# Kernel tuning notes

Hardware: AMD Instinct MI355X
Metric: run time of the kernel (lower is better)

Reference implementation:

```python
import jax, jax.numpy as jnp
import numpy as np

N = 50000   # nodes
E = 600000  # edges
D = 128     # in_channels == heads*hidden_channels
OUT = 64    # out_channels
L = 3       # local_layers
EPS = 1e-5  # BatchNorm eps


def setup_inputs() -> dict:
    key = jax.random.key(0)
    ks = jax.random.split(key, 10)
    s = 0.05
    x = jax.random.normal(ks[0], (N, D), jnp.float32)
    edge_index = jax.random.randint(ks[1], (2, E), 0, N, dtype=jnp.int32)
    Wg = jax.random.normal(ks[2], (L, D, D), jnp.float32) * s  # GCNConv weights
    bg = jnp.zeros((L, D), jnp.float32)                         # GCNConv biases
    Wl = jax.random.normal(ks[3], (L, D, D), jnp.float32) * s  # residual Linear weights
    bl = jax.random.normal(ks[4], (L, D), jnp.float32) * s
    gamma = jnp.ones((L, D), jnp.float32)                       # BN scale
    beta = jnp.zeros((L, D), jnp.float32)                       # BN shift
    Wp = jax.random.normal(ks[5], (D, OUT), jnp.float32) * s   # pred head
    bp = jnp.zeros((OUT,), jnp.float32)
    return {"x": x, "edge_index": edge_index, "Wg": Wg, "bg": bg,
            "Wl": Wl, "bl": bl, "gamma": gamma, "beta": beta,
            "Wp": Wp, "bp": bp}


def reference(x, edge_index, Wg, bg, Wl, bl, gamma, beta, Wp, bp):
    src, dst = edge_index[0], edge_index[1]
    # GCN symmetric normalization with self-loops (PyG gcn_norm):
    # deg computed on target (col) including self-loop.
    deg = jax.ops.segment_sum(jnp.ones((E,), x.dtype), dst, num_segments=N) + 1.0
    dinv = jax.lax.rsqrt(deg)                      # deg^{-1/2}, [N]
    enorm = dinv[src] * dinv[dst]                  # per-edge norm, [E]
    self_norm = (dinv * dinv)[:, None]             # deg^{-1} for self-loop, [N,1]

    h = x
    x_local = jnp.zeros((N, D), x.dtype)
    for i in range(L):
        hg = h @ Wg[i]                             # [N, D] transformed features
        # gather -> weight -> scatter-add (message passing) + self-loop term
        agg = jax.ops.segment_sum(hg[src] * enorm[:, None], dst, num_segments=N)
        conv = agg + hg * self_norm + bg[i]
        # residual linear
        h = conv + h @ Wl[i] + bl[i]
        # BatchNorm1d (training-mode batch statistics, biased var)
        mu = jnp.mean(h, axis=0)
        var = jnp.mean(jnp.square(h - mu), axis=0)
        h = (h - mu) * jax.lax.rsqrt(var + EPS) * gamma[i] + beta[i]
        h = jax.nn.relu(h)
        x_local = x_local + h                      # add_ accumulation
    return x_local @ Wp + bp
```

## Files before the change

kernel.cpp:

```cpp
#include <hip/hip_runtime.h>

#define D 128
#define OUTC 64
#define EC 256

typedef float floatx4 __attribute__((ext_vector_type(4)));
typedef short short8 __attribute__((ext_vector_type(8)));

__device__ inline unsigned short f2bf(float f) {
  unsigned int u = __float_as_uint(f);
  unsigned int r = (u + 0x7FFF + ((u >> 16) & 1)) >> 16;
  return (unsigned short)r;
}

__device__ inline int swz(int row, int k) { return row * 128 + (k ^ ((row & 7) << 3)); }

__global__ __launch_bounds__(256) void k_prepx(const float* __restrict__ x, unsigned short* __restrict__ xb, int total4) {
  int stride = gridDim.x * blockDim.x;
  for (int i = blockIdx.x * blockDim.x + threadIdx.x; i < total4; i += stride) {
    float4 v = ((const float4*)x)[i];
    ushort4 o;
    o.x = f2bf(v.x); o.y = f2bf(v.y); o.z = f2bf(v.z); o.w = f2bf(v.w);
    ((ushort4*)xb)[i] = o;
  }
}

__global__ __launch_bounds__(256) void k_prepw(const float* __restrict__ Wg, const float* __restrict__ Wl,
                                               const float* __restrict__ Wp,
                                               unsigned short* __restrict__ Wgt, unsigned short* __restrict__ Wlt,
                                               unsigned short* __restrict__ Wpt) {
  int u = blockIdx.x * 256 + threadIdx.x;
  const int W1 = 3 * D * D;
  if (u < W1) {
    int i = u / (D * D), rem = u % (D * D);
    int k = rem / D, n = rem % D;
    Wgt[i * D * D + n * D + k] = f2bf(Wg[u]);
  } else if (u < 2 * W1) {
    int v = u - W1;
    int i = v / (D * D), rem = v % (D * D);
    int k = rem / D, n = rem % D;
    Wlt[i * D * D + n * D + k] = f2bf(Wl[v]);
  } else if (u < 2 * W1 + D * OUTC) {
    int v = u - 2 * W1;
    int k = v / OUTC, n = v % OUTC;
    Wpt[n * D + k] = f2bf(Wp[v]);
  }
}


__global__ __launch_bounds__(256) void k_bh(const int* __restrict__ dst, int* __restrict__ bh,
                                            int E, int nbuk, int chk) {
  __shared__ int hist[256];
  int t = threadIdx.x, c = blockIdx.x;
  hist[t] = 0;
  __syncthreads();
  int s = c * chk, e = min(E, s + chk);
  for (int j = s + t; j < e; j += 256)
    atomicAdd(&hist[dst[j] >> 8], 1);
  __syncthreads();
  if (t < nbuk) bh[t * EC + c] = hist[t];
}

__device__ inline int block_scan4(int4 v, int t, int* total) {
  int s = v.x + v.y + v.z + v.w;
  int lane = t & 63, w = t >> 6;
  int incl = s;
  #pragma unroll
  for (int off = 1; off < 64; off <<= 1) {
    int nb = __shfl_up(incl, off);
    if (lane >= off) incl += nb;
  }
  __shared__ int wsum[4];
  if (lane == 63) wsum[w] = incl;
  __syncthreads();
  int woff = 0;
  #pragma unroll
  for (int k = 0; k < 3; ++k) if (w > k) woff += wsum[k];
  if (total) *total = wsum[0] + wsum[1] + wsum[2] + wsum[3];
  return woff + incl - s;
}

__global__ __launch_bounds__(256) void k_gscan1(int* __restrict__ arr, int* __restrict__ bsum, int n) {
  int t = threadIdx.x;
  int i0 = blockIdx.x * 1024 + t * 4;
  int4 v = make_int4(0, 0, 0, 0);
  if (i0 + 3 < n) v = *(const int4*)(arr + i0);
  else {
    if (i0 < n) v.x = arr[i0];
    if (i0 + 1 < n) v.y = arr[i0 + 1];
    if (i0 + 2 < n) v.z = arr[i0 + 2];
    if (i0 + 3 < n) v.w = arr[i0 + 3];
  }
  int total;
  int e = block_scan4(v, t, &total);
  if (i0 < n) {
    int4 o;
    o.x = e; o.y = e + v.x; o.z = o.y + v.y; o.w = o.z + v.z;
    if (i0 + 3 < n) *(int4*)(arr + i0) = o;
    else {
      arr[i0] = o.x;
      if (i0 + 1 < n) arr[i0 + 1] = o.y;
      if (i0 + 2 < n) arr[i0 + 2] = o.z;
    }
  }
  if (t == 0) bsum[blockIdx.x] = total;
}

__global__ __launch_bounds__(256) void k_gscan2(int* __restrict__ bsum, int nb) {
  int t = threadIdx.x;
  int i0 = t * 4;
  int4 v = make_int4(0, 0, 0, 0);
  if (i0 + 3 < nb) v = *(const int4*)(bsum + i0);
  else {
    if (i0 < nb) v.x = bsum[i0];
    if (i0 + 1 < nb) v.y = bsum[i0 + 1];
    if (i0 + 2 < nb) v.z = bsum[i0 + 2];
    if (i0 + 3 < nb) v.w = bsum[i0 + 3];
  }
  int e = block_scan4(v, t, nullptr);
  if (i0 < nb) {
    bsum[i0] = e;
    if (i0 + 1 < nb) bsum[i0 + 1] = e + v.x;
    if (i0 + 2 < nb) bsum[i0 + 2] = e + v.x + v.y;
    if (i0 + 3 < nb) bsum[i0 + 3] = e + v.x + v.y + v.z;
  }
}

__global__ __launch_bounds__(256) void k_scatter(const int* __restrict__ src, const int* __restrict__ dst,
                                                 const int* __restrict__ bhs, const int* __restrict__ bsum,
                                                 int2* __restrict__ ebuk, int E, int nbuk, int chk) {
  __shared__ int cur[256];
  int t = threadIdx.x, c = blockIdx.x;
  if (t < nbuk) {
    int idx = t * EC + c;
    cur[t] = bhs[idx] + bsum[idx >> 10];
  }
  __syncthreads();
  int s = c * chk, e = min(E, s + chk);
  for (int j = s + t; j < e; j += 256) {
    int d = dst[j];
    int pos = atomicAdd(&cur[d >> 8], 1);
    ebuk[pos] = make_int2(src[j], d);
  }
}

__global__ __launch_bounds__(256) void k_csr(const int2* __restrict__ ebuk, const int* __restrict__ bhs,
                                             const int* __restrict__ bsum,
                                             int* __restrict__ rowstart, int* __restrict__ csr,
                                             float* __restrict__ dinv, int E, int N, int nbuk) {
  __shared__ int cnt[256];
  __shared__ int wsum[4];
  int t = threadIdx.x, b = blockIdx.x;
  int si = b * EC;
  int s = bhs[si] + bsum[si >> 10];
  int e;
  if (b + 1 < nbuk) { int ei_ = (b + 1) * EC; e = bhs[ei_] + bsum[ei_ >> 10]; }
  else e = E;
  cnt[t] = 0;
  __syncthreads();
  for (int j = s + t; j < e; j += 256)
    atomicAdd(&cnt[ebuk[j].y & 255], 1);
  __syncthreads();
  int v = cnt[t];
  int lane = t & 63, w = t >> 6;
  int incl = v;
  #pragma unroll
  for (int off = 1; off < 64; off <<= 1) {
    int nb = __shfl_up(incl, off);
    if (lane >= off) incl += nb;
  }
  if (lane == 63) wsum[w] = incl;
  __syncthreads();
  int woff = 0;
  #pragma unroll
  for (int k = 0; k < 3; ++k) if (w > k) woff += wsum[k];
  int rs = s + woff + incl - v;
  int node = (b << 8) + t;
  __syncthreads();
  cnt[t] = rs;
  if (node < N) {
    rowstart[node] = rs;
    dinv[node] = rsqrtf((float)v + 1.0f);
  }
  if (node == 0) rowstart[N] = E;
  __syncthreads();
  for (int j = s + t; j < e; j += 256) {
    int2 ed = ebuk[j];
    int pos = atomicAdd(&cnt[ed.y & 255], 1);
    csr[pos] = ed.x;
  }
}

__global__ __launch_bounds__(256) void k_dual(const unsigned short* __restrict__ Ab,
                                              const unsigned short* __restrict__ Wgt,
                                              const unsigned short* __restrict__ Wlt,
                                              const float* __restrict__ bg, const float* __restrict__ bl,
                                              unsigned short* __restrict__ hg, float* __restrict__ hl, int M) {
  __shared__ unsigned short As[64 * 128];
  __shared__ unsigned short Bs[128 * 128];
  int tid = threadIdx.x;
  int row0 = blockIdx.x * 64;

  {
    int r = tid >> 2;
    int row = row0 + r;
    const unsigned short* src = Ab + (size_t)row * D;
    #pragma unroll
    for (int j = 0; j < 4; ++j) {
      int c = (tid & 3) + j * 4;
      short8 v = {0, 0, 0, 0, 0, 0, 0, 0};
      if (row < M) v = *(const short8*)(src + c * 8);
      *(short8*)&As[swz(r, c * 8)] = v;
    }
  }
  #pragma unroll
  for (int j = 0; j < 8; ++j) {
    int idx = tid + j * 256;
    int nr = idx >> 4, c = idx & 15;
    *(short8*)&Bs[swz(nr, c * 8)] = *(const short8*)(Wgt + nr * D + c * 8);
  }
  __syncthreads();

  int lane = tid & 63, w = tid >> 6;
  int lrow = lane & 15, lk = (lane >> 4) * 8;

  short8 af[4][4];
  #pragma unroll
  for (int m = 0; m < 4; ++m) {
    int ar = lrow + m * 16;
    #pragma unroll
    for (int kk = 0; kk < 4; ++kk)
      af[m][kk] = *(const short8*)&As[swz(ar, lk + kk * 32)];
  }

  {
    short8 bfg[2][4];
    #pragma unroll
    for (int n = 0; n < 2; ++n) {
      int br = w * 32 + n * 16 + lrow;
      #pragma unroll
      for (int kk = 0; kk < 4; ++kk)
        bfg[n][kk] = *(const short8*)&Bs[swz(br, lk + kk * 32)];
    }
    floatx4 acc[4][2];
    #pragma unroll
    for (int m = 0; m < 4; ++m)
      #pragma unroll
      for (int n = 0; n < 2; ++n)
        acc[m][n] = (floatx4)0.0f;
    #pragma unroll
    for (int kk = 0; kk < 4; ++kk)
      #pragma unroll
      for (int m = 0; m < 4; ++m)
        #pragma unroll
        for (int n = 0; n < 2; ++n)
          acc[m][n] = __builtin_amdgcn_mfma_f32_16x16x32_bf16(af[m][kk], bfg[n][kk], acc[m][n], 0, 0, 0);
    #pragma unroll
    for (int m = 0; m < 4; ++m)
      #pragma unroll
      for (int n = 0; n < 2; ++n) {
        int col = w * 32 + n * 16 + lrow;
        #pragma unroll
        for (int reg = 0; reg < 4; ++reg) {
          int row = row0 + m * 16 + (lane >> 4) * 4 + reg;
          if (row < M) hg[(size_t)row * D + col] = f2bf(acc[m][n][reg]);
        }
      }
  }
  __syncthreads();
  #pragma unroll
  for (int j = 0; j < 8; ++j) {
    int idx = tid + j * 256;
    int nr = idx >> 4, c = idx & 15;
    *(short8*)&Bs[swz(nr, c * 8)] = *(const short8*)(Wlt + nr * D + c * 8);
  }
  __syncthreads();
  {
    short8 bfl[2][4];
    #pragma unroll
    for (int n = 0; n < 2; ++n) {
      int br = w * 32 + n * 16 + lrow;
      #pragma unroll
      for (int kk = 0; kk < 4; ++kk)
        bfl[n][kk] = *(const short8*)&Bs[swz(br, lk + kk * 32)];
    }
    floatx4 acc[4][2];
    #pragma unroll
    for (int m = 0; m < 4; ++m)
      #pragma unroll
      for (int n = 0; n < 2; ++n)
        acc[m][n] = (floatx4)0.0f;
    #pragma unroll
    for (int kk = 0; kk < 4; ++kk)
      #pragma unroll
      for (int m = 0; m < 4; ++m)
        #pragma unroll
        for (int n = 0; n < 2; ++n)
          acc[m][n] = __builtin_amdgcn_mfma_f32_16x16x32_bf16(af[m][kk], bfl[n][kk], acc[m][n], 0, 0, 0);
    #pragma unroll
    for (int m = 0; m < 4; ++m)
      #pragma unroll
      for (int n = 0; n < 2; ++n) {
        int col = w * 32 + n * 16 + lrow;
        float bias = bg[col] + bl[col];
        #pragma unroll
        for (int reg = 0; reg < 4; ++reg) {
          int row = row0 + m * 16 + (lane >> 4) * 4 + reg;
          if (row < M) hl[(size_t)row * D + col] = acc[m][n][reg] + bias;
        }
      }
  }
}

__global__ __launch_bounds__(256) void k_agg(const unsigned short* __restrict__ hg, float* __restrict__ pre,
                                             const int* __restrict__ rowstart, const int* __restrict__ csr,
                                             const float* __restrict__ dinv,
                                             float* __restrict__ partial, int n, int ABS) {
  int t = threadIdx.x, b = blockIdx.x;
  int w = t >> 6, lane = t & 63;
  const unsigned int* base = (const unsigned int*)hg;
  float st_s0 = 0.f, st_s1 = 0.f, st_q0 = 0.f, st_q1 = 0.f;
  int c = lane * 2;
  int node0 = b * 16 + w * 4;
  #pragma unroll 1
  for (int k = 0; k < 4; ++k) {
    int node = node0 + k;
    if (node >= n) break;
    int s = rowstart[node], e = rowstart[node + 1];
    float dn = dinv[node];
    unsigned int ps = base[(size_t)node * 64 + lane];
    float* pp = pre + (size_t)node * D;
    float2 old = *(const float2*)(pp + c);
    float a0 = 0.f, a1 = 0.f, b0 = 0.f, b1 = 0.f;
    float c0 = 0.f, c1 = 0.f, d0 = 0.f, d1 = 0.f;
    int j = s;
    for (; j + 4 <= e; j += 4) {
      int sn0 = csr[j], sn1 = csr[j + 1], sn2 = csr[j + 2], sn3 = csr[j + 3];
      float w0 = dinv[sn0], w1 = dinv[sn1], w2 = dinv[sn2], w3 = dinv[sn3];
      unsigned int p0 = base[(size_t)sn0 * 64 + lane];
      unsigned int p1 = base[(size_t)sn1 * 64 + lane];
      unsigned int p2 = base[(size_t)sn2 * 64 + lane];
      unsigned int p3 = base[(size_t)sn3 * 64 + lane];
      a0 += w0 * __uint_as_float(p0 << 16); a1 += w0 * __uint_as_float(p0 & 0xFFFF0000u);
      b0 += w1 * __uint_as_float(p1 << 16); b1 += w1 * __uint_as_float(p1 & 0xFFFF0000u);
      c0 += w2 * __uint_as_float(p2 << 16); c1 += w2 * __uint_as_float(p2 & 0xFFFF0000u);
      d0 += w3 * __uint_as_float(p3 << 16); d1 += w3 * __uint_as_float(p3 & 0xFFFF0000u);
    }
    for (; j < e; ++j) {
      int sn = csr[j];
      float wv = dinv[sn];
      unsigned int p = base[(size_t)sn * 64 + lane];
      a0 += wv * __uint_as_float(p << 16);
      a1 += wv * __uint_as_float(p & 0xFFFF0000u);
    }
    float acc0 = (a0 + b0) + (c0 + d0);
    float acc1 = (a1 + b1) + (c1 + d1);
    float sf = dn * dn;
    float h0 = __uint_as_float(ps << 16);
    float h1 = __uint_as_float(ps & 0xFFFF0000u);
    float p0 = dn * acc0 + h0 * sf + old.x;
    float p1 = dn * acc1 + h1 * sf + old.y;
    *(float2*)(pp + c) = make_float2(p0, p1);
    st_s0 += p0; st_s1 += p1;
    st_q0 += p0 * p0; st_q1 += p1 * p1;
  }
  __shared__ float sm[4][128], sq[4][128];
  sm[w][c] = st_s0; sm[w][c + 1] = st_s1;
  sq[w][c] = st_q0; sq[w][c + 1] = st_q1;
  __syncthreads();
  if (t < 128) {
    float s = (sm[0][t] + sm[1][t]) + (sm[2][t] + sm[3][t]);
    float q = (sq[0][t] + sq[1][t]) + (sq[2][t] + sq[3][t]);
    partial[(size_t)t * ABS + b] = s;
    partial[(size_t)(128 + t) * ABS + b] = q;
  }
}

__global__ __launch_bounds__(256) void k_fin2(const float* __restrict__ partial,
                                              const float* __restrict__ gamma, const float* __restrict__ beta,
                                              float* __restrict__ ab, int nab, int ABS, float invN) {
  int cch = blockIdx.x;
  int t = threadIdx.x;
  const float* ps = partial + (size_t)cch * ABS;
  const float* pq = partial + (size_t)(128 + cch) * ABS;
  float s = 0.f, q = 0.f;
  for (int i = t; i < nab; i += 256) { s += ps[i]; q += pq[i]; }
  __shared__ float rs[256], rq[256];
  rs[t] = s; rq[t] = q;
  __syncthreads();
  if (t < 64) {
    s = (rs[t] + rs[t + 64]) + (rs[t + 128] + rs[t + 192]);
    q = (rq[t] + rq[t + 64]) + (rq[t + 128] + rq[t + 192]);
    #pragma unroll
    for (int off = 32; off; off >>= 1) {
      s += __shfl_down(s, off);
      q += __shfl_down(q, off);
    }
    if (t == 0) {
      float mean = s * invN;
      float var = q * invN - mean * mean;
      float inv = rsqrtf(var + 1e-5f);
      float g = gamma[cch];
      ab[cch] = g * inv;
      ab[128 + cch] = beta[cch] - mean * inv * g;
    }
  }
}

template<bool FIRST>
__global__ __launch_bounds__(256) void k_fused(const float* __restrict__ pre, const float* __restrict__ ab,
                                               const unsigned short* __restrict__ Wpt, const float* __restrict__ bp,
                                               const unsigned short* __restrict__ Wgt,
                                               const unsigned short* __restrict__ Wlt,
                                               const float* __restrict__ bgn, const float* __restrict__ bln,
                                               float* __restrict__ out, unsigned short* __restrict__ hg,
                                               float* __restrict__ hl, int M) {
  __shared__ unsigned short As[64 * 128];
  __shared__ unsigned short Bs[128 * 128];
  int tid = threadIdx.x;
  int row0 = blockIdx.x * 64;

  {
    int r = tid >> 2, qq = tid & 3;
    int row = row0 + r;
    bool valid = row < M;
    const float* Pp = pre + (size_t)row * D;
    #pragma unroll
    for (int ch = 0; ch < 4; ++ch) {
      int k0 = qq * 32 + ch * 8;
      float4 p0 = make_float4(0.f, 0.f, 0.f, 0.f), p1 = p0;
      if (valid) { p0 = *(const float4*)(Pp + k0); p1 = *(const float4*)(Pp + k0 + 4); }
      float4 a0 = *(const float4*)(ab + k0),        a1 = *(const float4*)(ab + k0 + 4);
      float4 b0 = *(const float4*)(ab + 128 + k0),  b1 = *(const float4*)(ab + 128 + k0 + 4);
      unsigned short hv[8];
      hv[0] = f2bf(fmaxf(p0.x * a0.x + b0.x, 0.f));
      hv[1] = f2bf(fmaxf(p0.y * a0.y + b0.y, 0.f));
      hv[2] = f2bf(fmaxf(p0.z * a0.z + b0.z, 0.f));
      hv[3] = f2bf(fmaxf(p0.w * a0.w + b0.w, 0.f));
      hv[4] = f2bf(fmaxf(p1.x * a1.x + b1.x, 0.f));
      hv[5] = f2bf(fmaxf(p1.y * a1.y + b1.y, 0.f));
      hv[6] = f2bf(fmaxf(p1.z * a1.z + b1.z, 0.f));
      hv[7] = f2bf(fmaxf(p1.w * a1.w + b1.w, 0.f));
      *(short8*)&As[swz(r, k0)] = *(const short8*)hv;
    }
  }
  #pragma unroll
  for (int j = 0; j < 4; ++j) {
    int idx = tid + j * 256;
    int nr = idx >> 4, c = idx & 15;
    *(short8*)&Bs[swz(nr, c * 8)] = *(const short8*)(Wpt + nr * D + c * 8);
  }
  __syncthreads();

  int lane = tid & 63, w = tid >> 6;
  int lrow = lane & 15, lk = (lane >> 4) * 8;

  short8 af[4][4];
  #pragma unroll
  for (int m = 0; m < 4; ++m) {
    int ar = lrow + m * 16;
    #pragma unroll
    for (int kk = 0; kk < 4; ++kk)
      af[m][kk] = *(const short8*)&As[swz(ar, lk + kk * 32)];
  }

  {
    short8 bfr[4];
    int br = w * 16 + lrow;
    #pragma unroll
    for (int kk = 0; kk < 4; ++kk)
      bfr[kk] = *(const short8*)&Bs[swz(br, lk + kk * 32)];
    floatx4 acc[4];
    #pragma unroll
    for (int m = 0; m < 4; ++m) acc[m] = (floatx4)0.0f;
    #pragma unroll
    for (int kk = 0; kk < 4; ++kk)
      #pragma unroll
      for (int m = 0; m < 4; ++m)
        acc[m] = __builtin_amdgcn_mfma_f32_16x16x32_bf16(af[m][kk], bfr[kk], acc[m], 0, 0, 0);
    int col = w * 16 + lrow;
    float bpv = FIRST ? bp[col] : 0.f;
    #pragma unroll
    for (int m = 0; m < 4; ++m)
      #pragma unroll
      for (int reg = 0; reg < 4; ++reg) {
        int row = row0 + m * 16 + (lane >> 4) * 4 + reg;
        if (row < M) {
          float* op = &out[(size_t)row * OUTC + col];
          float v = acc[m][reg] + bpv;
          if (!FIRST) v += *op;
          *op = v;
        }
      }
  }
  __syncthreads();
  #pragma unroll
  for (int j = 0; j < 8; ++j) {
    int idx = tid + j * 256;
    int nr = idx >> 4, c = idx & 15;
    *(short8*)&Bs[swz(nr, c * 8)] = *(const short8*)(Wgt + nr * D + c * 8);
  }
  __syncthreads();
  {
    short8 bfg[2][4];
    #pragma unroll
    for (int n = 0; n < 2; ++n) {
      int br = w * 32 + n * 16 + lrow;
      #pragma unroll
      for (int kk = 0; kk < 4; ++kk)
        bfg[n][kk] = *(const short8*)&Bs[swz(br, lk + kk * 32)];
    }
    floatx4 acc[4][2];
    #pragma unroll
    for (int m = 0; m < 4; ++m)
      #pragma unroll
      for (int n = 0; n < 2; ++n)
        acc[m][n] = (floatx4)0.0f;
    #pragma unroll
    for (int kk = 0; kk < 4; ++kk)
      #pragma unroll
      for (int m = 0; m < 4; ++m)
        #pragma unroll
        for (int n = 0; n < 2; ++n)
          acc[m][n] = __builtin_amdgcn_mfma_f32_16x16x32_bf16(af[m][kk], bfg[n][kk], acc[m][n], 0, 0, 0);
    #pragma unroll
    for (int m = 0; m < 4; ++m)
      #pragma unroll
      for (int n = 0; n < 2; ++n) {
        int col = w * 32 + n * 16 + lrow;
        #pragma unroll
        for (int reg = 0; reg < 4; ++reg) {
          int row = row0 + m * 16 + (lane >> 4) * 4 + reg;
          if (row < M) hg[(size_t)row * D + col] = f2bf(acc[m][n][reg]);
        }
      }
  }
  __syncthreads();
  #pragma unroll
  for (int j = 0; j < 8; ++j) {
    int idx = tid + j * 256;
    int nr = idx >> 4, c = idx & 15;
    *(short8*)&Bs[swz(nr, c * 8)] = *(const short8*)(Wlt + nr * D + c * 8);
  }
  __syncthreads();
  {
    short8 bfl[2][4];
    #pragma unroll
    for (int n = 0; n < 2; ++n) {
      int br = w * 32 + n * 16 + lrow;
      #pragma unroll
      for (int kk = 0; kk < 4; ++kk)
        bfl[n][kk] = *(const short8*)&Bs[swz(br, lk + kk * 32)];
    }
    floatx4 acc[4][2];
    #pragma unroll
    for (int m = 0; m < 4; ++m)
      #pragma unroll
      for (int n = 0; n < 2; ++n)
        acc[m][n] = (floatx4)0.0f;
    #pragma unroll
    for (int kk = 0; kk < 4; ++kk)
      #pragma unroll
      for (int m = 0; m < 4; ++m)
        #pragma unroll
        for (int n = 0; n < 2; ++n)
          acc[m][n] = __builtin_amdgcn_mfma_f32_16x16x32_bf16(af[m][kk], bfl[n][kk], acc[m][n], 0, 0, 0);
    #pragma unroll
    for (int m = 0; m < 4; ++m)
      #pragma unroll
      for (int n = 0; n < 2; ++n) {
        int col = w * 32 + n * 16 + lrow;
        float bias = bgn[col] + bln[col];
        #pragma unroll
        for (int reg = 0; reg < 4; ++reg) {
          int row = row0 + m * 16 + (lane >> 4) * 4 + reg;
          if (row < M) hl[(size_t)row * D + col] = acc[m][n][reg] + bias;
        }
      }
  }
}

__global__ __launch_bounds__(256) void k_out(const float* __restrict__ pre, const float* __restrict__ ab,
                                             const unsigned short* __restrict__ Wpt,
                                             float* __restrict__ out, int M) {
  __shared__ unsigned short As[64 * 128];
  __shared__ unsigned short Bs[OUTC * 128];
  int tid = threadIdx.x;
  int row0 = blockIdx.x * 64;

  {
    int r = tid >> 2, qq = tid & 3;
    int row = row0 + r;
    bool valid = row < M;
    const float* Pp = pre + (size_t)row * D;
    #pragma unroll
    for (int ch = 0; ch < 4; ++ch) {
      int k0 = qq * 32 + ch * 8;
      float4 p0 = make_float4(0.f, 0.f, 0.f, 0.f), p1 = p0;
      if (valid) { p0 = *(const float4*)(Pp + k0); p1 = *(const float4*)(Pp + k0 + 4); }
      float4 a0 = *(const float4*)(ab + k0),        a1 = *(const float4*)(ab + k0 + 4);
      float4 b0 = *(const float4*)(ab + 128 + k0),  b1 = *(const float4*)(ab + 128 + k0 + 4);
      unsigned short hv[8];
      hv[0] = f2bf(fmaxf(p0.x * a0.x + b0.x, 0.f));
      hv[1] = f2bf(fmaxf(p0.y * a0.y + b0.y, 0.f));
      hv[2] = f2bf(fmaxf(p0.z * a0.z + b0.z, 0.f));
      hv[3] = f2bf(fmaxf(p0.w * a0.w + b0.w, 0.f));
      hv[4] = f2bf(fmaxf(p1.x * a1.x + b1.x, 0.f));
      hv[5] = f2bf(fmaxf(p1.y * a1.y + b1.y, 0.f));
      hv[6] = f2bf(fmaxf(p1.z * a1.z + b1.z, 0.f));
      hv[7] = f2bf(fmaxf(p1.w * a1.w + b1.w, 0.f));
      *(short8*)&As[swz(r, k0)] = *(const short8*)hv;
    }
  }
  #pragma unroll
  for (int j = 0; j < 4; ++j) {
    int idx = tid + j * 256;
    int nr = idx >> 4, c = idx & 15;
    *(short8*)&Bs[swz(nr, c * 8)] = *(const short8*)(Wpt + nr * D + c * 8);
  }
  __syncthreads();

  int lane = tid & 63, w = tid >> 6;
  int lrow = lane & 15, lk = (lane >> 4) * 8;

  short8 af[4][4];
  #pragma unroll
  for (int m = 0; m < 4; ++m) {
    int ar = lrow + m * 16;
    #pragma unroll
    for (int kk = 0; kk < 4; ++kk)
      af[m][kk] = *(const short8*)&As[swz(ar, lk + kk * 32)];
  }
  short8 bfr[4];
  {
    int br = w * 16 + lrow;
    #pragma unroll
    for (int kk = 0; kk < 4; ++kk)
      bfr[kk] = *(const short8*)&Bs[swz(br, lk + kk * 32)];
  }
  floatx4 acc[4];
  #pragma unroll
  for (int m = 0; m < 4; ++m) acc[m] = (floatx4)0.0f;
  #pragma unroll
  for (int kk = 0; kk < 4; ++kk)
    #pragma unroll
    for (int m = 0; m < 4; ++m)
      acc[m] = __builtin_amdgcn_mfma_f32_16x16x32_bf16(af[m][kk], bfr[kk], acc[m], 0, 0, 0);

  int col = w * 16 + lrow;
  #pragma unroll
  for (int m = 0; m < 4; ++m)
    #pragma unroll
    for (int reg = 0; reg < 4; ++reg) {
      int row = row0 + m * 16 + (lane >> 4) * 4 + reg;
      if (row < M) {
        float* op = &out[(size_t)row * OUTC + col];
        *op = *op + acc[m][reg];
      }
    }
}

extern "C" void kernel_launch(void* const* d_in, const int* in_sizes, int n_in,
                              void* d_out, int out_size, void* d_ws, size_t ws_size,
                              hipStream_t stream) {
  const float* x     = (const float*)d_in[0];
  const int*   ei    = (const int*)d_in[1];
  const float* Wg    = (const float*)d_in[2];
  const float* bg    = (const float*)d_in[3];
  const float* Wl    = (const float*)d_in[4];
  const float* bl    = (const float*)d_in[5];
  const float* gamma = (const float*)d_in[6];
  const float* beta  = (const float*)d_in[7];
  const float* Wp    = (const float*)d_in[8];
  const float* bp    = (const float*)d_in[9];
  float* out = (float*)d_out;

  int N = in_sizes[0] / D;
  int E = in_sizes[1] / 2;
  const int* srcp = ei;
  const int* dstp = ei + E;

  char* wsb = (char*)d_ws;
  size_t off = 0;
  auto alloc = [&](size_t bytes) {
    off = (off + 255) & ~(size_t)255;
    void* p = wsb + off;
    off += bytes;
    return p;
  };
  int nab = (N + 15) / 16;
  int ABS = (nab + 63) & ~63;
  float* dinv     = (float*)alloc((size_t)N * 4);
  int*   rowstart = (int*)alloc((size_t)(N + 1) * 4);
  int*   csr      = (int*)alloc((size_t)E * 4);
  int*   bh       = (int*)alloc((size_t)256 * EC * 4);
  int2*  ebuk     = (int2*)alloc((size_t)E * 8);
  int*   bsum     = (int*)alloc(1024 * 4);
  float* partial  = (float*)alloc((size_t)256 * ABS * 4);
  float* ab       = (float*)alloc(3 * 256 * 4);
  unsigned short* xb  = (unsigned short*)alloc((size_t)N * D * 2);
  unsigned short* hg  = (unsigned short*)alloc((size_t)N * D * 2);
  float* hl       = (float*)alloc((size_t)N * D * 4);
  unsigned short* Wgt = (unsigned short*)alloc(3 * D * D * 2);
  unsigned short* Wlt = (unsigned short*)alloc(3 * D * D * 2);
  unsigned short* Wpt = (unsigned short*)alloc(D * OUTC * 2);
  (void)ws_size; (void)n_in; (void)out_size;

  k_prepx<<<1024, 256, 0, stream>>>(x, xb, N * D / 4);
  int wtotal = 2 * 3 * D * D + D * OUTC;
  k_prepw<<<(wtotal + 255) / 256, 256, 0, stream>>>(Wg, Wl, Wp, Wgt, Wlt, Wpt);

  int nbuk = (N + 255) >> 8;
  int chk  = (E + EC - 1) / EC;
  k_bh<<<EC, 256, 0, stream>>>(dstp, bh, E, nbuk, chk);
  int sn  = nbuk * EC;
  int snb = (sn + 1023) >> 10;
  k_gscan1<<<snb, 256, 0, stream>>>(bh, bsum, sn);
  k_gscan2<<<1, 256, 0, stream>>>(bsum, snb);
  k_scatter<<<EC, 256, 0, stream>>>(srcp, dstp, bh, bsum, ebuk, E, nbuk, chk);
  k_csr<<<nbuk, 256, 0, stream>>>(ebuk, bh, bsum, rowstart, csr, dinv, E, N, nbuk);

  int mt = (N + 63) / 64;
  float invN = 1.0f / (float)N;

  k_dual<<<mt, 256, 0, stream>>>(xb, Wgt, Wlt, bg, bl, hg, hl, N);

  for (int i = 0; i < 3; ++i) {
    k_agg<<<nab, 256, 0, stream>>>(hg, hl, rowstart, csr, dinv, partial, N, ABS);
    k_fin2<<<128, 256, 0, stream>>>(partial, gamma + (size_t)i * D, beta + (size_t)i * D,
                                    ab + i * 256, nab, ABS, invN);
    if (i == 0)
      k_fused<true><<<mt, 256, 0, stream>>>(hl, ab + i * 256, Wpt, bp,
                                            Wgt + (size_t)(i + 1) * D * D, Wlt + (size_t)(i + 1) * D * D,
                                            bg + (size_t)(i + 1) * D, bl + (size_t)(i + 1) * D,
                                            out, hg, hl, N);
    else if (i == 1)
      k_fused<false><<<mt, 256, 0, stream>>>(hl, ab + i * 256, Wpt, bp,
                                             Wgt + (size_t)(i + 1) * D * D, Wlt + (size_t)(i + 1) * D * D,
                                             bg + (size_t)(i + 1) * D, bl + (size_t)(i + 1) * D,
                                             out, hg, hl, N);
    else
      k_out<<<mt, 256, 0, stream>>>(hl, ab + i * 256, Wpt, out, N);
  }
}
```

Measured before the change: 290.8 us.

## Store residual/pre-activation buffer in bf16 and pack edge buckets into 32-bit words

The residual-linear output buffer (hl/pre) is now stored as bf16 instead of fp32, halving its traffic in the dual GEMM epilogue, the aggregation read-modify-write, and the fused/out prologues. Edge bucket entries are packed into a single 32-bit word (24-bit src plus 8-bit local dst), halving scatter/CSR-build traffic. The aggregation kernel handles 2 nodes per wave instead of 4, doubling the block count. Risks: extra rounding in the pre-BN activations, and src indices are limited to 24 bits.

```diff
diff --git a/kernel.cpp b/kernel.cpp
--- a/kernel.cpp
+++ b/kernel.cpp
@@ -11,6 +11,9 @@
   unsigned int u = __float_as_uint(f);
   unsigned int r = (u + 0x7FFF + ((u >> 16) & 1)) >> 16;
   return (unsigned short)r;
+}
+__device__ inline float bf2f(unsigned short u) {
+  return __uint_as_float(((unsigned int)u) << 16);
 }
 
 __device__ inline int swz(int row, int k) { return row * 128 + (k ^ ((row & 7) << 3)); }
@@ -128,7 +131,7 @@
 
 __global__ __launch_bounds__(256) void k_scatter(const int* __restrict__ src, const int* __restrict__ dst,
                                                  const int* __restrict__ bhs, const int* __restrict__ bsum,
-                                                 int2* __restrict__ ebuk, int E, int nbuk, int chk) {
+                                                 unsigned int* __restrict__ ebuk, int E, int nbuk, int chk) {
   __shared__ int cur[256];
   int t = threadIdx.x, c = blockIdx.x;
   if (t < nbuk) {
@@ -140,11 +143,11 @@
   for (int j = s + t; j < e; j += 256) {
     int d = dst[j];
     int pos = atomicAdd(&cur[d >> 8], 1);
-    ebuk[pos] = make_int2(src[j], d);
-  }
-}
-
-__global__ __launch_bounds__(256) void k_csr(const int2* __restrict__ ebuk, const int* __restrict__ bhs,
+    ebuk[pos] = (unsigned int)src[j] | ((unsigned int)(d & 255) << 24);
+  }
+}
+
+__global__ __launch_bounds__(256) void k_csr(const unsigned int* __restrict__ ebuk, const int* __restrict__ bhs,
                                              const int* __restrict__ bsum,
                                              int* __restrict__ rowstart, int* __restrict__ csr,
                                              float* __restrict__ dinv, int E, int N, int nbuk) {
@@ -159,7 +162,7 @@
   cnt[t] = 0;
   __syncthreads();
   for (int j = s + t; j < e; j += 256)
-    atomicAdd(&cnt[ebuk[j].y & 255], 1);
+    atomicAdd(&cnt[ebuk[j] >> 24], 1);
   __syncthreads();
   int v = cnt[t];
   int lane = t & 63, w = t >> 6;
@@ -185,9 +188,9 @@
   if (node == 0) rowstart[N] = E;
   __syncthreads();
   for (int j = s + t; j < e; j += 256) {
-    int2 ed = ebuk[j];
-    int pos = atomicAdd(&cnt[ed.y & 255], 1);
-    csr[pos] = ed.x;
+    unsigned int ed = ebuk[j];
+    int pos = atomicAdd(&cnt[ed >> 24], 1);
+    csr[pos] = (int)(ed & 0xFFFFFFu);
   }
 }
 
@@ -195,7 +198,7 @@
                                               const unsigned short* __restrict__ Wgt,
                                               const unsigned short* __restrict__ Wlt,
                                               const float* __restrict__ bg, const float* __restrict__ bl,
-                                              unsigned short* __restrict__ hg, float* __restrict__ hl, int M) {
+                                              unsigned short* __restrict__ hg, unsigned short* __restrict__ hl, int M) {
   __shared__ unsigned short As[64 * 128];
   __shared__ unsigned short Bs[128 * 128];
   int tid = threadIdx.x;
@@ -306,31 +309,31 @@
         #pragma unroll
         for (int reg = 0; reg < 4; ++reg) {
           int row = row0 + m * 16 + (lane >> 4) * 4 + reg;
-          if (row < M) hl[(size_t)row * D + col] = acc[m][n][reg] + bias;
+          if (row < M) hl[(size_t)row * D + col] = f2bf(acc[m][n][reg] + bias);
         }
       }
   }
 }
 
-__global__ __launch_bounds__(256) void k_agg(const unsigned short* __restrict__ hg, float* __restrict__ pre,
+__global__ __launch_bounds__(256) void k_agg(const unsigned short* __restrict__ hg, unsigned short* __restrict__ pre,
                                              const int* __restrict__ rowstart, const int* __restrict__ csr,
                                              const float* __restrict__ dinv,
                                              float* __restrict__ partial, int n, int ABS) {
   int t = threadIdx.x, b = blockIdx.x;
   int w = t >> 6, lane = t & 63;
   const unsigned int* base = (const unsigned int*)hg;
+  unsigned int* prew = (unsigned int*)pre;
   float st_s0 = 0.f, st_s1 = 0.f, st_q0 = 0.f, st_q1 = 0.f;
   int c = lane * 2;
-  int node0 = b * 16 + w * 4;
+  int node0 = b * 8 + w * 2;
   #pragma unroll 1
-  for (int k = 0; k < 4; ++k) {
+  for (int k = 0; k < 2; ++k) {
     int node = node0 + k;
     if (node >= n) break;
     int s = rowstart[node], e = rowstart[node + 1];
     float dn = dinv[node];
     unsigned int ps = base[(size_t)node * 64 + lane];
-    float* pp = pre + (size_t)node * D;
-    float2 old = *(const float2*)(pp + c);
+    unsigned int oldw = prew[(size_t)node * 64 + lane];
     float a0 = 0.f, a1 = 0.f, b0 = 0.f, b1 = 0.f;
     float c0 = 0.f, c1 = 0.f, d0 = 0.f, d1 = 0.f;
     int j = s;
@@ -358,9 +361,11 @@
     float sf = dn * dn;
     float h0 = __uint_as_float(ps << 16);
     float h1 = __uint_as_float(ps & 0xFFFF0000u);
-    float p0 = dn * acc0 + h0 * sf + old.x;
-    float p1 = dn * acc1 + h1 * sf + old.y;
-    *(float2*)(pp + c) = make_float2(p0, p1);
+    float old0 = __uint_as_float(oldw << 16);
+    float old1 = __uint_as_float(oldw & 0xFFFF0000u);
+    float p0 = dn * acc0 + h0 * sf + old0;
+    float p1 = dn * acc1 + h1 * sf + old1;
+    prew[(size_t)node * 64 + lane] = (unsigned int)f2bf(p0) | ((unsigned int)f2bf(p1) << 16);
     st_s0 += p0; st_s1 += p1;
     st_q0 += p0 * p0; st_q1 += p1 * p1;
   }
@@ -408,13 +413,13 @@
 }
 
 template<bool FIRST>
-__global__ __launch_bounds__(256) void k_fused(const float* __restrict__ pre, const float* __restrict__ ab,
+__global__ __launch_bounds__(256) void k_fused(const unsigned short* __restrict__ pre, const float* __restrict__ ab,
                                                const unsigned short* __restrict__ Wpt, const float* __restrict__ bp,
                                                const unsigned short* __restrict__ Wgt,
                                                const unsigned short* __restrict__ Wlt,
                                                const float* __restrict__ bgn, const float* __restrict__ bln,
                                                float* __restrict__ out, unsigned short* __restrict__ hg,
-                                               float* __restrict__ hl, int M) {
+                                               unsigned short* __restrict__ hl, int M) {
   __shared__ unsigned short As[64 * 128];
   __shared__ unsigned short Bs[128 * 128];
   int tid = threadIdx.x;
@@ -424,23 +429,22 @@
     int r = tid >> 2, qq = tid & 3;
     int row = row0 + r;
     bool valid = row < M;
-    const float* Pp = pre + (size_t)row * D;
+    const unsigned short* Pp = pre + (size_t)row * D;
     #pragma unroll
     for (int ch = 0; ch < 4; ++ch) {
       int k0 = qq * 32 + ch * 8;
-      float4 p0 = make_float4(0.f, 0.f, 0.f, 0.f), p1 = p0;
-      if (valid) { p0 = *(const float4*)(Pp + k0); p1 = *(const float4*)(Pp + k0 + 4); }
+      short8 pv = {0, 0, 0, 0, 0, 0, 0, 0};
+      if (valid) pv = *(const short8*)(Pp + k0);
       float4 a0 = *(const float4*)(ab + k0),        a1 = *(const float4*)(ab + k0 + 4);
       float4 b0 = *(const float4*)(ab + 128 + k0),  b1 = *(const float4*)(ab + 128 + k0 + 4);
+      float av[8] = {a0.x, a0.y, a0.z, a0.w, a1.x, a1.y, a1.z, a1.w};
+      float bv[8] = {b0.x, b0.y, b0.z, b0.w, b1.x, b1.y, b1.z, b1.w};
       unsigned short hv[8];
-      hv[0] = f2bf(fmaxf(p0.x * a0.x + b0.x, 0.f));
-      hv[1] = f2bf(fmaxf(p0.y * a0.y + b0.y, 0.f));
-      hv[2] = f2bf(fmaxf(p0.z * a0.z + b0.z, 0.f));
-      hv[3] = f2bf(fmaxf(p0.w * a0.w + b0.w, 0.f));
-      hv[4] = f2bf(fmaxf(p1.x * a1.x + b1.x, 0.f));
-      hv[5] = f2bf(fmaxf(p1.y * a1.y + b1.y, 0.f));
-      hv[6] = f2bf(fmaxf(p1.z * a1.z + b1.z, 0.f));
-      hv[7] = f2bf(fmaxf(p1.w * a1.w + b1.w, 0.f));
+      #pragma unroll
+      for (int jj = 0; jj < 8; ++jj) {
+        float f = bf2f((unsigned short)pv[jj]);
+        hv[jj] = f2bf(fmaxf(f * av[jj] + bv[jj], 0.f));
+      }
       *(short8*)&As[swz(r, k0)] = *(const short8*)hv;
     }
   }
@@ -574,13 +578,13 @@
         #pragma unroll
         for (int reg = 0; reg < 4; ++reg) {
           int row = row0 + m * 16 + (lane >> 4) * 4 + reg;
-          if (row < M) hl[(size_t)row * D + col] = acc[m][n][reg] + bias;
+          if (row < M) hl[(size_t)row * D + col] = f2bf(acc[m][n][reg] + bias);
         }
       }
   }
 }
 
-__global__ __launch_bounds__(256) void k_out(const float* __restrict__ pre, const float* __restrict__ ab,
+__global__ __launch_bounds__(256) void k_out(const unsigned short* __restrict__ pre, const float* __restrict__ ab,
                                              const unsigned short* __restrict__ Wpt,
                                              float* __restrict__ out, int M) {
   __shared__ unsigned short As[64 * 128];
@@ -592,23 +596,22 @@
     int r = tid >> 2, qq = tid & 3;
     int row = row0 + r;
     bool valid = row < M;
-    const float* Pp = pre + (size_t)row * D;
+    const unsigned short* Pp = pre + (size_t)row * D;
     #pragma unroll
     for (int ch = 0; ch < 4; ++ch) {
       int k0 = qq * 32 + ch * 8;
-      float4 p0 = make_float4(0.f, 0.f, 0.f, 0.f), p1 = p0;
-      if (valid) { p0 = *(const float4*)(Pp + k0); p1 = *(const float4*)(Pp + k0 + 4); }
+      short8 pv = {0, 0, 0, 0, 0, 0, 0, 0};
+      if (valid) pv = *(const short8*)(Pp + k0);
       float4 a0 = *(const float4*)(ab + k0),        a1 = *(const float4*)(ab + k0 + 4);
       float4 b0 = *(const float4*)(ab + 128 + k0),  b1 = *(const float4*)(ab + 128 + k0 + 4);
+      float av[8] = {a0.x, a0.y, a0.z, a0.w, a1.x, a1.y, a1.z, a1.w};
+      float bv[8] = {b0.x, b0.y, b0.z, b0.w, b1.x, b1.y, b1.z, b1.w};
       unsigned short hv[8];
-      hv[0] = f2bf(fmaxf(p0.x * a0.x + b0.x, 0.f));
-      hv[1] = f2bf(fmaxf(p0.y * a0.y + b0.y, 0.f));
-      hv[2] = f2bf(fmaxf(p0.z * a0.z + b0.z, 0.f));
-      hv[3] = f2bf(fmaxf(p0.w * a0.w + b0.w, 0.f));
-      hv[4] = f2bf(fmaxf(p1.x * a1.x + b1.x, 0.f));
-      hv[5] = f2bf(fmaxf(p1.y * a1.y + b1.y, 0.f));
-      hv[6] = f2bf(fmaxf(p1.z * a1.z + b1.z, 0.f));
-      hv[7] = f2bf(fmaxf(p1.w * a1.w + b1.w, 0.f));
+      #pragma unroll
+      for (int jj = 0; jj < 8; ++jj) {
+        float f = bf2f((unsigned short)pv[jj]);
+        hv[jj] = f2bf(fmaxf(f * av[jj] + bv[jj], 0.f));
+      }
       *(short8*)&As[swz(r, k0)] = *(const short8*)hv;
     }
   }
@@ -688,19 +691,19 @@
     off += bytes;
     return p;
   };
-  int nab = (N + 15) / 16;
+  int nab = (N + 7) / 8;
   int ABS = (nab + 63) & ~63;
   float* dinv     = (float*)alloc((size_t)N * 4);
   int*   rowstart = (int*)alloc((size_t)(N + 1) * 4);
   int*   csr      = (int*)alloc((size_t)E * 4);
   int*   bh       = (int*)alloc((size_t)256 * EC * 4);
-  int2*  ebuk     = (int2*)alloc((size_t)E * 8);
+  unsigned int* ebuk = (unsigned int*)alloc((size_t)E * 4);
   int*   bsum     = (int*)alloc(1024 * 4);
   float* partial  = (float*)alloc((size_t)256 * ABS * 4);
   float* ab       = (float*)alloc(3 * 256 * 4);
   unsigned short* xb  = (unsigned short*)alloc((size_t)N * D * 2);
   unsigned short* hg  = (unsigned short*)alloc((size_t)N * D * 2);
-  float* hl       = (float*)alloc((size_t)N * D * 4);
+  unsigned short* hl  = (unsigned short*)alloc((size_t)N * D * 2);
   unsigned short* Wgt = (unsigned short*)alloc(3 * D * D * 2);
   unsigned short* Wlt = (unsigned short*)alloc(3 * D * D * 2);
   unsigned short* Wpt = (unsigned short*)alloc(D * OUTC * 2);
```

New measurement: 299.7 us. 3.1% more time.
